# Optimization experiments

Measured on AMD Instinct MI355X. Metric: run time of the kernel, lower is better.

The kernel has to match this reference:

```python
import jax, jax.numpy as jnp
import numpy as np

# Domain bounds and training nu-range (from init_kwargs)
X_MIN, X_MAX = -1.0, 1.0
Y_MIN, Y_MAX = -1.0, 1.0
T_MIN, T_MAX = 0.0, 1.0
NU_MIN, NU_MAX = 0.01, 0.1

LAYERS = [4, 256, 256, 256, 256, 2]
N = 16384  # collocation points


def setup_inputs() -> dict:
    key = jax.random.key(0)
    ks = jax.random.split(key, 4 + 2 * (len(LAYERS) - 1))
    inp = {
        'x': jax.random.uniform(ks[0], (N, 1), minval=X_MIN, maxval=X_MAX, dtype=jnp.float32),
        'y': jax.random.uniform(ks[1], (N, 1), minval=Y_MIN, maxval=Y_MAX, dtype=jnp.float32),
        't': jax.random.uniform(ks[2], (N, 1), minval=T_MIN, maxval=T_MAX, dtype=jnp.float32),
        'nu': jax.random.uniform(ks[3], (N, 1), minval=NU_MIN, maxval=NU_MAX, dtype=jnp.float32),
    }
    # glorot_normal weights, zero biases (keras Dense defaults)
    for i in range(len(LAYERS) - 1):
        fan_in, fan_out = LAYERS[i], LAYERS[i + 1]
        std = (2.0 / (fan_in + fan_out)) ** 0.5
        inp[f'W{i}'] = std * jax.random.normal(ks[4 + 2 * i], (fan_in, fan_out), dtype=jnp.float32)
        inp[f'b{i}'] = jnp.zeros((fan_out,), dtype=jnp.float32)
    return inp


def _net(pt, nu, params):
    """MLP forward for a single point. pt: (3,) = (x, y, t); nu: scalar. Returns (2,) = (u, v)."""
    x, y, t = pt[0], pt[1], pt[2]
    h = jnp.stack([
        2.0 * (x - X_MIN) / (X_MAX - X_MIN) - 1.0,
        2.0 * (y - Y_MIN) / (Y_MAX - Y_MIN) - 1.0,
        2.0 * (t - T_MIN) / (T_MAX - T_MIN) - 1.0,
        2.0 * (nu - NU_MIN) / (NU_MAX - NU_MIN) - 1.0,
    ])
    for W, b in params[:-1]:
        z = h @ W + b
        h = z * jax.nn.sigmoid(z)  # swish
    W, b = params[-1]
    return h @ W + b


def _residual_point(pt, nu, params):
    """Burgers PDE residual (f_u, f_v) at one collocation point via nested forward-mode AD."""
    f = lambda p: _net(p, nu, params)
    uv = f(pt)                          # (2,)
    J = jax.jacfwd(f)(pt)               # (2,3): d(u,v)/d(x,y,t)
    H = jax.jacfwd(jax.jacfwd(f))(pt)   # (2,3,3)
    u, v = uv[0], uv[1]
    u_x, u_y, u_t = J[0, 0], J[0, 1], J[0, 2]
    v_x, v_y, v_t = J[1, 0], J[1, 1], J[1, 2]
    u_xx, u_yy = H[0, 0, 0], H[0, 1, 1]
    v_xx, v_yy = H[1, 0, 0], H[1, 1, 1]
    f_u = u_t + u * u_x + v * u_y - nu * (u_xx + u_yy)
    f_v = v_t + u * v_x + v * v_y - nu * (v_xx + v_yy)
    return jnp.stack([f_u, f_v])


def reference(x, y, t, nu, W0, b0, W1, b1, W2, b2, W3, b3, W4, b4):
    params = [(W0, b0), (W1, b1), (W2, b2), (W3, b3), (W4, b4)]
    pts = jnp.concatenate([x, y, t], axis=1)  # (N, 3)
    res = jax.vmap(lambda p, n: _residual_point(p, n, params))(pts, nu[:, 0])
    return res  # (N, 2) = [f_u, f_v]
```

## Files before the change

### kernel.cpp

```cpp
#include <hip/hip_runtime.h>

typedef _Float16 f16;
typedef _Float16 v8hf __attribute__((ext_vector_type(8)));
typedef _Float16 v4hf __attribute__((ext_vector_type(4)));
typedef _Float16 v2hf __attribute__((ext_vector_type(2)));
typedef float    v4f  __attribute__((ext_vector_type(4)));

#define NPTS 16384
#define PTS  8
#define LDA  264
#define NLAYER_ELEMS 65536

__global__ void pack_weights(const float* __restrict__ W1, const float* __restrict__ W2,
                             const float* __restrict__ W3, f16* __restrict__ bh,
                             f16* __restrict__ bl) {
    const int L = blockIdx.x >> 3, ks = blockIdx.x & 7, n = threadIdx.x;
    const float* W = (L == 0) ? W1 : (L == 1) ? W2 : W3;
    f16 h[32], l[32];
    #pragma unroll
    for (int kk = 0; kk < 32; ++kk) {
        float w = W[(ks * 32 + kk) * 256 + n];
        f16 hh = (f16)w;
        h[kk] = hh;
        l[kk] = (f16)(w - (float)hh);
    }
    size_t off = (size_t)L * NLAYER_ELEMS + (size_t)(ks * 256 + n) * 32;
    #pragma unroll
    for (int i = 0; i < 4; ++i) {
        *(v8hf*)(bh + off + 8 * i) = *(v8hf*)(h + 8 * i);
        *(v8hf*)(bl + off + 8 * i) = *(v8hf*)(l + 8 * i);
    }
}

__global__ __launch_bounds__(256, 3) void pinn_burgers_kernel(
    const float* __restrict__ gx, const float* __restrict__ gy,
    const float* __restrict__ gt, const float* __restrict__ gnu,
    const float* __restrict__ W0, const float* __restrict__ b0,
    const float* __restrict__ b1, const float* __restrict__ b2,
    const float* __restrict__ b3,
    const float* __restrict__ W4, const float* __restrict__ b4,
    const f16* __restrict__ bh, const f16* __restrict__ bl,
    float* __restrict__ out)
{
    __shared__ f16 Ah[48 * LDA];
    __shared__ f16 Al[48 * LDA];
    __shared__ float red[PTS][12];
    __shared__ float pin[4][PTS];

    const int tid  = threadIdx.x;
    const int lane = tid & 63;
    const int wv   = tid >> 6;
    const int ln   = lane & 15;
    const int quad = lane >> 4;
    const int p0   = blockIdx.x * PTS;

    if (tid < 4 * PTS) {
        int c = tid >> 3, p = tid & 7;
        const float* src = (c == 0) ? gx : (c == 1) ? gy : (c == 2) ? gt : gnu;
        pin[c][p] = src[p0 + p];
    }
    __syncthreads();

    {
        const int jp = tid & 127, j0 = jp * 2, pg = tid >> 7;
        float w00[2], w01[2], w02[2], w03[2], bb[2];
        #pragma unroll
        for (int e = 0; e < 2; ++e) {
            int j = j0 + e;
            w00[e] = W0[j]; w01[e] = W0[256 + j]; w02[e] = W0[512 + j]; w03[e] = W0[768 + j];
            bb[e] = b0[j];
        }
        #pragma unroll
        for (int pp = 0; pp < 4; ++pp) {
            int p = pg * 4 + pp;
            float hx = pin[0][p];
            float hy = pin[1][p];
            float ht = 2.f * pin[2][p] - 1.f;
            float hn = 2.f * (pin[3][p] - 0.01f) * (1.f / 0.09f) - 1.f;
            float a[6][2];
            #pragma unroll
            for (int e = 0; e < 2; ++e) {
                float z  = hx * w00[e] + hy * w01[e] + ht * w02[e] + hn * w03[e] + bb[e];
                float zx = w00[e], zy = w01[e], zt = 2.f * w02[e];
                float s  = 1.f / (1.f + __expf(-z));
                float g1 = s + z * s * (1.f - s);
                float g2 = s * (1.f - s) * (2.f + z * (1.f - 2.f * s));
                a[0][e] = z * s;
                a[1][e] = g1 * zx; a[2][e] = g1 * zy; a[3][e] = g1 * zt;
                a[4][e] = g2 * zx * zx; a[5][e] = g2 * zy * zy;
            }
            #pragma unroll
            for (int c = 0; c < 6; ++c) {
                v2hf hh = { (f16)a[c][0], (f16)a[c][1] };
                v2hf ll = { (f16)(a[c][0] - (float)hh[0]), (f16)(a[c][1] - (float)hh[1]) };
                *(v2hf*)&Ah[(c * PTS + p) * LDA + j0] = hh;
                *(v2hf*)&Al[(c * PTS + p) * LDA + j0] = ll;
            }
        }
    }
    __syncthreads();

    const float* bias_ptr[3] = { b1, b2, b3 };
    for (int L = 0; L < 3; ++L) {
        const f16* __restrict__ bhL = bh + (size_t)L * NLAYER_ELEMS;
        const f16* __restrict__ blL = bl + (size_t)L * NLAYER_ELEMS;
        const float* __restrict__ bv = bias_ptr[L];

        v4f acc[4][3];
        #pragma unroll
        for (int t = 0; t < 4; ++t)
            #pragma unroll
            for (int mt = 0; mt < 3; ++mt)
                acc[t][mt] = (v4f){0.f, 0.f, 0.f, 0.f};

        #pragma unroll 2
        for (int ks = 0; ks < 8; ++ks) {
            v8hf a_h[3], a_l[3];
            #pragma unroll
            for (int mt = 0; mt < 3; ++mt) {
                const f16* p = Ah + (mt * 16 + ln) * LDA + ks * 32 + quad * 8;
                a_h[mt] = *(const v8hf*)p;
                a_l[mt] = *(const v8hf*)(p + 48 * LDA);
            }
            #pragma unroll
            for (int mt = 0; mt < 3; ++mt) {
                const f16* p = Al + (mt * 16 + ln) * LDA + ks * 32 + quad * 8;
                a_l[mt] = *(const v8hf*)p;
            }
            v8hf w_h[4], w_l[4];
            #pragma unroll
            for (int t = 0; t < 4; ++t) {
                int n = wv * 64 + t * 16 + ln;
                size_t o = (size_t)(ks * 256 + n) * 32 + quad * 8;
                w_h[t] = *(const v8hf*)(bhL + o);
                w_l[t] = *(const v8hf*)(blL + o);
            }
            #pragma unroll
            for (int t = 0; t < 4; ++t)
                #pragma unroll
                for (int mt = 0; mt < 3; ++mt) {
                    acc[t][mt] = __builtin_amdgcn_mfma_f32_16x16x32_f16(w_h[t], a_h[mt], acc[t][mt], 0, 0, 0);
                    acc[t][mt] = __builtin_amdgcn_mfma_f32_16x16x32_f16(w_h[t], a_l[mt], acc[t][mt], 0, 0, 0);
                    acc[t][mt] = __builtin_amdgcn_mfma_f32_16x16x32_f16(w_l[t], a_h[mt], acc[t][mt], 0, 0, 0);
                }
        }
        __syncthreads();

        #pragma unroll
        for (int t = 0; t < 4; ++t)
            #pragma unroll
            for (int mt = 0; mt < 3; ++mt) {
                v4f a = acc[t][mt];
                int nb = wv * 64 + t * 16 + quad * 4;
                int m  = mt * 16 + ln;
                if (mt == 0 && ln < PTS) {
                    const float4 bq = *(const float4*)(bv + nb);
                    a[0] += bq.x; a[1] += bq.y; a[2] += bq.z; a[3] += bq.w;
                }
                v4hf hi = { (f16)a[0], (f16)a[1], (f16)a[2], (f16)a[3] };
                v4hf lo = { (f16)(a[0] - (float)hi[0]), (f16)(a[1] - (float)hi[1]),
                            (f16)(a[2] - (float)hi[2]), (f16)(a[3] - (float)hi[3]) };
                *(v4hf*)&Ah[m * LDA + nb] = hi;
                *(v4hf*)&Al[m * LDA + nb] = lo;
            }
        __syncthreads();

        {
            const int jp = tid & 127, j0 = jp * 2, pg = tid >> 7;
            #pragma unroll
            for (int pp = 0; pp < 4; ++pp) {
                int p = pg * 4 + pp;
                float z[6][2];
                #pragma unroll
                for (int c = 0; c < 6; ++c) {
                    v2hf hh = *(v2hf*)&Ah[(c * PTS + p) * LDA + j0];
                    v2hf ll = *(v2hf*)&Al[(c * PTS + p) * LDA + j0];
                    z[c][0] = (float)hh[0] + (float)ll[0];
                    z[c][1] = (float)hh[1] + (float)ll[1];
                }
                float a[6][2];
                #pragma unroll
                for (int e = 0; e < 2; ++e) {
                    float zz = z[0][e];
                    float s  = 1.f / (1.f + __expf(-zz));
                    float g1 = s + zz * s * (1.f - s);
                    float g2 = s * (1.f - s) * (2.f + zz * (1.f - 2.f * s));
                    a[0][e] = zz * s;
                    a[1][e] = g1 * z[1][e];
                    a[2][e] = g1 * z[2][e];
                    a[3][e] = g1 * z[3][e];
                    a[4][e] = g2 * z[1][e] * z[1][e] + g1 * z[4][e];
                    a[5][e] = g2 * z[2][e] * z[2][e] + g1 * z[5][e];
                }
                #pragma unroll
                for (int c = 0; c < 6; ++c) {
                    v2hf hh = { (f16)a[c][0], (f16)a[c][1] };
                    v2hf ll = { (f16)(a[c][0] - (float)hh[0]), (f16)(a[c][1] - (float)hh[1]) };
                    *(v2hf*)&Ah[(c * PTS + p) * LDA + j0] = hh;
                    *(v2hf*)&Al[(c * PTS + p) * LDA + j0] = ll;
                }
            }
        }
        __syncthreads();
    }

    #pragma unroll
    for (int d = 0; d < 24; ++d) {
        int D  = wv * 24 + d;
        int p  = D / 12;
        int rm = D % 12;
        int c  = rm >> 1;
        int o  = rm & 1;
        int m  = c * PTS + p;
        int k0 = lane * 4;
        v4hf hh = *(v4hf*)&Ah[m * LDA + k0];
        v4hf ll = *(v4hf*)&Al[m * LDA + k0];
        float partial = 0.f;
        #pragma unroll
        for (int i = 0; i < 4; ++i)
            partial += ((float)hh[i] + (float)ll[i]) * W4[(k0 + i) * 2 + o];
        #pragma unroll
        for (int off = 32; off > 0; off >>= 1)
            partial += __shfl_down(partial, off);
        if (lane == 0)
            red[p][rm] = partial + ((c == 0) ? b4[o] : 0.f);
    }
    __syncthreads();

    if (tid < PTS) {
        int p = tid;
        float u   = red[p][0],  v   = red[p][1];
        float ux  = red[p][2],  vx  = red[p][3];
        float uy  = red[p][4],  vy  = red[p][5];
        float ut  = red[p][6],  vt  = red[p][7];
        float uxx = red[p][8],  vxx = red[p][9];
        float uyy = red[p][10], vyy = red[p][11];
        float nuv = pin[3][p];
        float fu = ut + u * ux + v * uy - nuv * (uxx + uyy);
        float fv = vt + u * vx + v * vy - nuv * (vxx + vyy);
        out[(p0 + p) * 2 + 0] = fu;
        out[(p0 + p) * 2 + 1] = fv;
    }
}

extern "C" void kernel_launch(void* const* d_in, const int* in_sizes, int n_in,
                              void* d_out, int out_size, void* d_ws, size_t ws_size,
                              hipStream_t stream) {
    const float* x  = (const float*)d_in[0];
    const float* y  = (const float*)d_in[1];
    const float* t  = (const float*)d_in[2];
    const float* nu = (const float*)d_in[3];
    const float* W0 = (const float*)d_in[4];
    const float* b0 = (const float*)d_in[5];
    const float* W1 = (const float*)d_in[6];
    const float* b1 = (const float*)d_in[7];
    const float* W2 = (const float*)d_in[8];
    const float* b2 = (const float*)d_in[9];
    const float* W3 = (const float*)d_in[10];
    const float* b3 = (const float*)d_in[11];
    const float* W4 = (const float*)d_in[12];
    const float* b4 = (const float*)d_in[13];
    float* o = (float*)d_out;

    f16* bh = (f16*)d_ws;
    f16* bl = bh + 3 * (size_t)NLAYER_ELEMS;

    hipLaunchKernelGGL(pack_weights, dim3(24), dim3(256), 0, stream, W1, W2, W3, bh, bl);
    hipLaunchKernelGGL(pinn_burgers_kernel, dim3(NPTS / PTS), dim3(256), 0, stream,
                       x, y, t, nu, W0, b0, b1, b2, b3, W4, b4, bh, bl, o);
}
```

Baseline: 223.5 us.

## Swizzle LDS activation layout and drop an intra-layer barrier via wave-local columns

```diff
diff --git a/kernel.cpp b/kernel.cpp
--- a/kernel.cpp
+++ b/kernel.cpp
@@ -8,8 +8,11 @@
 
 #define NPTS 16384
 #define PTS  8
-#define LDA  264
 #define NLAYER_ELEMS 65536
+
+__device__ __forceinline__ int swz(int m, int j) {
+    return m * 256 + ((((j >> 3) ^ (m & 7)) << 3) | (j & 7));
+}
 
 __global__ void pack_weights(const float* __restrict__ W1, const float* __restrict__ W2,
                              const float* __restrict__ W3, f16* __restrict__ bh,
@@ -42,8 +45,8 @@
     const f16* __restrict__ bh, const f16* __restrict__ bl,
     float* __restrict__ out)
 {
-    __shared__ f16 Ah[48 * LDA];
-    __shared__ f16 Al[48 * LDA];
+    __shared__ f16 Ah[48 * 256];
+    __shared__ f16 Al[48 * 256];
     __shared__ float red[PTS][12];
     __shared__ float pin[4][PTS];
 
@@ -52,6 +55,7 @@
     const int wv   = tid >> 6;
     const int ln   = lane & 15;
     const int quad = lane >> 4;
+    const int lnx  = ln & 7;
     const int p0   = blockIdx.x * PTS;
 
     if (tid < 4 * PTS) {
@@ -61,8 +65,11 @@
     }
     __syncthreads();
 
+    const int l5 = lane & 31;
+    const int j0 = wv * 64 + l5 * 2;
+    const int ph = (lane >> 5) * 4;
+
     {
-        const int jp = tid & 127, j0 = jp * 2, pg = tid >> 7;
         float w00[2], w01[2], w02[2], w03[2], bb[2];
         #pragma unroll
         for (int e = 0; e < 2; ++e) {
@@ -72,7 +79,7 @@
         }
         #pragma unroll
         for (int pp = 0; pp < 4; ++pp) {
-            int p = pg * 4 + pp;
+            int p = ph + pp;
             float hx = pin[0][p];
             float hy = pin[1][p];
             float ht = 2.f * pin[2][p] - 1.f;
@@ -91,10 +98,11 @@
             }
             #pragma unroll
             for (int c = 0; c < 6; ++c) {
+                int idx = swz(c * PTS + p, j0);
                 v2hf hh = { (f16)a[c][0], (f16)a[c][1] };
                 v2hf ll = { (f16)(a[c][0] - (float)hh[0]), (f16)(a[c][1] - (float)hh[1]) };
-                *(v2hf*)&Ah[(c * PTS + p) * LDA + j0] = hh;
-                *(v2hf*)&Al[(c * PTS + p) * LDA + j0] = ll;
+                *(v2hf*)&Ah[idx] = hh;
+                *(v2hf*)&Al[idx] = ll;
             }
         }
     }
@@ -115,17 +123,13 @@
 
         #pragma unroll 2
         for (int ks = 0; ks < 8; ++ks) {
+            const int cb = (((4 * ks + quad) ^ lnx) << 3);
             v8hf a_h[3], a_l[3];
             #pragma unroll
             for (int mt = 0; mt < 3; ++mt) {
-                const f16* p = Ah + (mt * 16 + ln) * LDA + ks * 32 + quad * 8;
-                a_h[mt] = *(const v8hf*)p;
-                a_l[mt] = *(const v8hf*)(p + 48 * LDA);
-            }
-            #pragma unroll
-            for (int mt = 0; mt < 3; ++mt) {
-                const f16* p = Al + (mt * 16 + ln) * LDA + ks * 32 + quad * 8;
-                a_l[mt] = *(const v8hf*)p;
+                const int rb = (mt * 16 + ln) * 256 + cb;
+                a_h[mt] = *(const v8hf*)&Ah[rb];
+                a_l[mt] = *(const v8hf*)&Al[rb];
             }
             v8hf w_h[4], w_l[4];
             #pragma unroll
@@ -160,21 +164,21 @@
                 v4hf hi = { (f16)a[0], (f16)a[1], (f16)a[2], (f16)a[3] };
                 v4hf lo = { (f16)(a[0] - (float)hi[0]), (f16)(a[1] - (float)hi[1]),
                             (f16)(a[2] - (float)hi[2]), (f16)(a[3] - (float)hi[3]) };
-                *(v4hf*)&Ah[m * LDA + nb] = hi;
-                *(v4hf*)&Al[m * LDA + nb] = lo;
-            }
-        __syncthreads();
+                int idx = swz(m, nb);
+                *(v4hf*)&Ah[idx] = hi;
+                *(v4hf*)&Al[idx] = lo;
+            }
 
         {
-            const int jp = tid & 127, j0 = jp * 2, pg = tid >> 7;
             #pragma unroll
             for (int pp = 0; pp < 4; ++pp) {
-                int p = pg * 4 + pp;
+                int p = ph + pp;
                 float z[6][2];
                 #pragma unroll
                 for (int c = 0; c < 6; ++c) {
-                    v2hf hh = *(v2hf*)&Ah[(c * PTS + p) * LDA + j0];
-                    v2hf ll = *(v2hf*)&Al[(c * PTS + p) * LDA + j0];
+                    int idx = swz(c * PTS + p, j0);
+                    v2hf hh = *(v2hf*)&Ah[idx];
+                    v2hf ll = *(v2hf*)&Al[idx];
                     z[c][0] = (float)hh[0] + (float)ll[0];
                     z[c][1] = (float)hh[1] + (float)ll[1];
                 }
@@ -194,10 +198,11 @@
                 }
                 #pragma unroll
                 for (int c = 0; c < 6; ++c) {
+                    int idx = swz(c * PTS + p, j0);
                     v2hf hh = { (f16)a[c][0], (f16)a[c][1] };
                     v2hf ll = { (f16)(a[c][0] - (float)hh[0]), (f16)(a[c][1] - (float)hh[1]) };
-                    *(v2hf*)&Ah[(c * PTS + p) * LDA + j0] = hh;
-                    *(v2hf*)&Al[(c * PTS + p) * LDA + j0] = ll;
+                    *(v2hf*)&Ah[idx] = hh;
+                    *(v2hf*)&Al[idx] = ll;
                 }
             }
         }
@@ -213,8 +218,9 @@
         int o  = rm & 1;
         int m  = c * PTS + p;
         int k0 = lane * 4;
-        v4hf hh = *(v4hf*)&Ah[m * LDA + k0];
-        v4hf ll = *(v4hf*)&Al[m * LDA + k0];
+        int idx = swz(m, k0);
+        v4hf hh = *(v4hf*)&Ah[idx];
+        v4hf ll = *(v4hf*)&Al[idx];
         float partial = 0.f;
         #pragma unroll
         for (int i = 0; i < 4; ++i)
```

Result: no change. 221.2 us (-1.0%).
